# Kernel tuning notes

Hardware: AMD Instinct MI355X
Metric: run time of the kernel (lower is better)

The kernel has to match this reference:

```python
import jax, jax.numpy as jnp
import numpy as np

B, T, D, H, UNITS = 32, 2048, 512, 512, 512

def setup_inputs() -> dict:
    key = jax.random.key(0)
    ks = jax.random.split(key, 5)
    scale = 0.02
    return {
        "features": jax.random.normal(ks[0], (B, T, D), dtype=jnp.float32),
        "hidden": jax.random.normal(ks[1], (B, H), dtype=jnp.float32),
        "Wk": jax.random.normal(ks[2], (D, UNITS), dtype=jnp.float32) * scale,
        "Wb": jnp.zeros((UNITS,), dtype=jnp.float32),
        "Uk": jax.random.normal(ks[3], (H, UNITS), dtype=jnp.float32) * scale,
        "Ub": jnp.zeros((UNITS,), dtype=jnp.float32),
        "Vk": jax.random.normal(ks[4], (UNITS, 1), dtype=jnp.float32) * scale,
        "Vb": jnp.zeros((1,), dtype=jnp.float32),
    }

def reference(features, hidden, Wk, Wb, Uk, Ub, Vk, Vb):
    # features: [B, T, D], hidden: [B, H]
    wf = jnp.einsum('btd,du->btu', features, Wk) + Wb          # [B, T, U]
    uh = (hidden @ Uk + Ub)[:, None, :]                        # [B, 1, U]
    score = jnp.tanh(wf + uh)                                  # [B, T, U]
    logits = jnp.einsum('btu,uo->bto', score, Vk) + Vb         # [B, T, 1]
    attention_weights = jax.nn.softmax(logits, axis=1)         # [B, T, 1]
    context_vector = jnp.sum(attention_weights * features, axis=1)  # [B, D]
    return context_vector, attention_weights
```

## Files before the change

### kernel.cpp

```cpp
#include <hip/hip_runtime.h>
#include <stdint.h>


typedef unsigned short ushort_t;
typedef __attribute__((ext_vector_type(8))) short short8;
typedef __attribute__((ext_vector_type(4))) float f32x4;
typedef __attribute__((ext_vector_type(2))) float float2v;
typedef __attribute__((ext_vector_type(2))) __bf16 bf162v;

#define GLOBAL_AS __attribute__((address_space(1)))
#define LDS_AS    __attribute__((address_space(3)))

__device__ __forceinline__ ushort_t f2bf(float f) {
    uint32_t u = __builtin_bit_cast(uint32_t, f);
    u = (u + 0x7fffu + ((u >> 16) & 1u)) >> 16;
    return (ushort_t)u;
}
__device__ __forceinline__ float bf2f(ushort_t h) {
    uint32_t u = ((uint32_t)h) << 16;
    return __builtin_bit_cast(float, u);
}
__device__ __forceinline__ uint32_t pkbf(float a, float b) {
    bf162v r = __builtin_convertvector((float2v){a, b}, bf162v);
    return __builtin_bit_cast(uint32_t, r);
}

__global__ __launch_bounds__(256) void prep_all(
    const float* __restrict__ feats, ushort_t* __restrict__ fbf,
    const float* __restrict__ hidden, const float* __restrict__ Uk,
    const float* __restrict__ Ub, const float* __restrict__ Wb,
    const float* __restrict__ Wk,
    float* __restrict__ uh, ushort_t* __restrict__ WkT,
    float* __restrict__ ctx_out)
{
    if (blockIdx.x < 16384) {
        const size_t i = ((size_t)blockIdx.x * 256 + threadIdx.x) * 8;
        f32x4 a = *(const f32x4*)(feats + i);
        f32x4 b = *(const f32x4*)(feats + i + 4);
        union { short8 s; uint32_t u[4]; } r;
        r.u[0] = pkbf(a.x, a.y); r.u[1] = pkbf(a.z, a.w);
        r.u[2] = pkbf(b.x, b.y); r.u[3] = pkbf(b.z, b.w);
        *(short8*)(fbf + i) = r.s;
        return;
    }
    const int pb = blockIdx.x - 16384;
    if (pb < 256) {
        const int b  = pb >> 3;
        const int u  = (pb & 7) * 64 + (threadIdx.x & 63);
        const int k0 = (threadIdx.x >> 6) * 128;
        const float* hr = hidden + b * 512;
        float acc = 0.f;
        #pragma unroll 8
        for (int k = k0; k < k0 + 128; ++k)
            acc += hr[k] * Uk[k * 512 + u];
        __shared__ float red[256];
        red[threadIdx.x] = acc;
        __syncthreads();
        if (threadIdx.x < 64) {
            const int ul = threadIdx.x;
            uh[b * 512 + u] = red[ul] + red[ul + 64] + red[ul + 128] + red[ul + 192]
                            + Ub[u] + Wb[u];
        }
    } else if (pb < 512) {
        __shared__ float t[32][33];
        const int blk = pb - 256;
        const int ti = blk >> 4;
        const int tj = blk & 15;
        const int tx = threadIdx.x & 31;
        const int ty = threadIdx.x >> 5;
        #pragma unroll
        for (int q = 0; q < 4; ++q) {
            const int r = ty * 4 + q;
            t[r][tx] = Wk[(ti * 32 + r) * 512 + tj * 32 + tx];
        }
        __syncthreads();
        #pragma unroll
        for (int q = 0; q < 4; ++q) {
            const int r = ty * 4 + q;
            WkT[(tj * 32 + r) * 512 + ti * 32 + tx] = f2bf(t[tx][r]);
        }
    } else {
        ctx_out[(pb - 512) * 256 + threadIdx.x] = 0.f;
    }
}

template<bool CONV>
__global__ __launch_bounds__(512, 4) void attn_gemm(
    const float* __restrict__ afp, const ushort_t* __restrict__ abf,
    const ushort_t* __restrict__ WkT, const float* __restrict__ uh,
    const float* __restrict__ Vk, float* __restrict__ lg4)
{
    __shared__ __align__(16) short As[256 * 32];
    __shared__ __align__(16) short Bs[128 * 32];
    __shared__ float uh_s[128];
    __shared__ float vk_s[128];
    __shared__ float lpart[2][256];

    const int tid  = threadIdx.x;
    const int lane = tid & 63;
    const int quad = lane >> 4;
    const int lc   = lane & 15;
    const int wave = tid >> 6;
    const int wm   = wave >> 1;
    const int wn   = wave & 1;
    const int nc   = (blockIdx.x >> 7) & 3;
    const int mtile= (blockIdx.x & 127) | ((blockIdx.x >> 9) << 7);
    const int m0   = mtile * 256;
    const int bidx = m0 >> 11;

    if (tid < 128) {
        uh_s[tid] = uh[bidx * 512 + nc * 128 + tid];
        vk_s[tid] = Vk[nc * 128 + tid];
    }

    f32x4 acc[4][4];
    #pragma unroll
    for (int tm = 0; tm < 4; ++tm)
        #pragma unroll
        for (int tn = 0; tn < 4; ++tn)
            acc[tm][tn] = (f32x4){0.f, 0.f, 0.f, 0.f};

    for (int ks = 0; ks < 16; ++ks) {
        const int k0 = ks * 32;
        __syncthreads();
        {
            const int row = tid >> 2;
            const int kq  = (tid & 3) * 8;
            const ushort_t* gb = WkT + (size_t)(nc * 128 + row) * 512 + k0 + kq;
            __builtin_amdgcn_global_load_lds(
                (const GLOBAL_AS void*)gb, (LDS_AS void*)(Bs + tid * 8), 16, 0, 0);
        }
        if constexpr (CONV) {
            const int row = tid >> 1;
            const int k16 = (tid & 1) * 16;
            const float* ga = afp + (size_t)(m0 + row) * 512 + k0 + k16;
            f32x4 a0 = *(const f32x4*)(ga);
            f32x4 a1 = *(const f32x4*)(ga + 4);
            f32x4 a2 = *(const f32x4*)(ga + 8);
            f32x4 a3 = *(const f32x4*)(ga + 12);
            union { short8 s; uint32_t u[4]; } r0, r1;
            r0.u[0] = pkbf(a0.x, a0.y); r0.u[1] = pkbf(a0.z, a0.w);
            r0.u[2] = pkbf(a1.x, a1.y); r0.u[3] = pkbf(a1.z, a1.w);
            r1.u[0] = pkbf(a2.x, a2.y); r1.u[1] = pkbf(a2.z, a2.w);
            r1.u[2] = pkbf(a3.x, a3.y); r1.u[3] = pkbf(a3.z, a3.w);
            *(short8*)(As + row * 32 + k16)     = r0.s;
            *(short8*)(As + row * 32 + k16 + 8) = r1.s;
        } else {
            #pragma unroll
            for (int rnd = 0; rnd < 2; ++rnd) {
                const int li  = rnd * 512 + tid;
                const int row = li >> 2;
                const int kq  = (li & 3) * 8;
                const ushort_t* ga = abf + (size_t)(m0 + row) * 512 + k0 + kq;
                __builtin_amdgcn_global_load_lds(
                    (const GLOBAL_AS void*)ga, (LDS_AS void*)(As + li * 8), 16, 0, 0);
            }
        }
        __syncthreads();

        short8 af[4], bfr[4];
        #pragma unroll
        for (int t4 = 0; t4 < 4; ++t4) {
            af[t4]  = *(const short8*)(As + (wm * 64 + t4 * 16 + lc) * 32 + quad * 8);
            bfr[t4] = *(const short8*)(Bs + (wn * 64 + t4 * 16 + lc) * 32 + quad * 8);
        }
        #pragma unroll
        for (int tm = 0; tm < 4; ++tm)
            #pragma unroll
            for (int tn = 0; tn < 4; ++tn)
                acc[tm][tn] = __builtin_amdgcn_mfma_f32_16x16x32_bf16(
                    af[tm], bfr[tn], acc[tm][tn], 0, 0, 0);
    }

    float rp[16];
    #pragma unroll
    for (int i = 0; i < 16; ++i) rp[i] = 0.f;
    #pragma unroll
    for (int tn = 0; tn < 4; ++tn) {
        const int nl  = wn * 64 + tn * 16 + lc;
        const float uhv = uh_s[nl];
        const float vkv = vk_s[nl];
        #pragma unroll
        for (int tm = 0; tm < 4; ++tm)
            #pragma unroll
            for (int i = 0; i < 4; ++i) {
                const float x = acc[tm][tn][i] + uhv;
                const float e = __expf(2.0f * x);
                rp[tm * 4 + i] += (1.0f - 2.0f / (e + 1.0f)) * vkv;
            }
    }
    #pragma unroll
    for (int i = 0; i < 16; ++i) {
        float v = rp[i];
        v += __shfl_xor(v, 1, 64);
        v += __shfl_xor(v, 2, 64);
        v += __shfl_xor(v, 4, 64);
        v += __shfl_xor(v, 8, 64);
        rp[i] = v;
    }
    if (lc == 0) {
        #pragma unroll
        for (int tm = 0; tm < 4; ++tm)
            #pragma unroll
            for (int i = 0; i < 4; ++i)
                lpart[wn][wm * 64 + tm * 16 + quad * 4 + i] = rp[tm * 4 + i];
    }
    __syncthreads();
    if (tid < 256)
        lg4[(size_t)nc * 65536 + m0 + tid] = lpart[0][tid] + lpart[1][tid];
}

__global__ __launch_bounds__(256) void softmax_k(
    const float* __restrict__ lg4, float* __restrict__ aw_out)
{
    const int b = blockIdx.x, tid = threadIdx.x;
    const float* p = lg4 + b * 2048;
    float v[8];
    #pragma unroll
    for (int i = 0; i < 8; ++i) {
        const int idx = tid + i * 256;
        v[i] = p[idx] + p[idx + 65536] + p[idx + 131072] + p[idx + 196608];
    }
    float mx = -1e30f;
    #pragma unroll
    for (int i = 0; i < 8; ++i) mx = fmaxf(mx, v[i]);
    #pragma unroll
    for (int off = 32; off >= 1; off >>= 1) mx = fmaxf(mx, __shfl_xor(mx, off, 64));
    __shared__ float redm[4], reds[4];
    const int wv = tid >> 6, ln = tid & 63;
    if (ln == 0) redm[wv] = mx;
    __syncthreads();
    mx = fmaxf(fmaxf(redm[0], redm[1]), fmaxf(redm[2], redm[3]));
    float s = 0.f;
    #pragma unroll
    for (int i = 0; i < 8; ++i) { v[i] = __expf(v[i] - mx); s += v[i]; }
    #pragma unroll
    for (int off = 32; off >= 1; off >>= 1) s += __shfl_xor(s, off, 64);
    if (ln == 0) reds[wv] = s;
    __syncthreads();
    s = reds[0] + reds[1] + reds[2] + reds[3];
    const float inv = 1.0f / s;
    #pragma unroll
    for (int i = 0; i < 8; ++i)
        aw_out[b * 2048 + tid + i * 256] = v[i] * inv;
}

template<bool BF>
__global__ __launch_bounds__(256) void context_k(
    const ushort_t* __restrict__ fb, const float* __restrict__ ff,
    const float* __restrict__ aw, float* __restrict__ ctx_out)
{
    const int b  = blockIdx.x >> 4;
    const int t0 = (blockIdx.x & 15) * 128 + (threadIdx.x >> 7) * 64;
    const int d4 = (threadIdx.x & 127) * 4;
    const float* wp = aw + b * 2048 + t0;
    f32x4 a = (f32x4){0.f, 0.f, 0.f, 0.f};
    if constexpr (BF) {
        const ushort_t* fp = fb + (size_t)(b * 2048 + t0) * 512 + d4;
        #pragma unroll 4
        for (int tt = 0; tt < 64; ++tt) {
            const float w = wp[tt];
            union { uint2 u2; ushort_t h[4]; } r;
            r.u2 = *(const uint2*)(fp + (size_t)tt * 512);
            a.x += w * bf2f(r.h[0]); a.y += w * bf2f(r.h[1]);
            a.z += w * bf2f(r.h[2]); a.w += w * bf2f(r.h[3]);
        }
    } else {
        const float* fp = ff + (size_t)(b * 2048 + t0) * 512 + d4;
        #pragma unroll 4
        for (int tt = 0; tt < 64; ++tt) {
            const float w = wp[tt];
            const f32x4 f = *(const f32x4*)(fp + (size_t)tt * 512);
            a.x += w * f.x; a.y += w * f.y; a.z += w * f.z; a.w += w * f.w;
        }
    }
    atomicAdd(&ctx_out[b * 512 + d4],     a.x);
    atomicAdd(&ctx_out[b * 512 + d4 + 1], a.y);
    atomicAdd(&ctx_out[b * 512 + d4 + 2], a.z);
    atomicAdd(&ctx_out[b * 512 + d4 + 3], a.w);
}

extern "C" void kernel_launch(void* const* d_in, const int* in_sizes, int n_in,
                              void* d_out, int out_size, void* d_ws, size_t ws_size,
                              hipStream_t stream)
{
    const float* feats  = (const float*)d_in[0];
    const float* hidden = (const float*)d_in[1];
    const float* Wk     = (const float*)d_in[2];
    const float* Wb     = (const float*)d_in[3];
    const float* Uk     = (const float*)d_in[4];
    const float* Ub     = (const float*)d_in[5];
    const float* Vk     = (const float*)d_in[6];

    float* out       = (float*)d_out;
    float* ctx_out_p = out;
    float* aw_out_p  = out + 16384;

    char* ws = (char*)d_ws;
    float*    uh  = (float*)ws;
    ushort_t* WkT = (ushort_t*)(ws + 65536);
    float*    lg4 = (float*)(ws + 589824);
    ushort_t* fbf = (ushort_t*)(ws + (2u << 20));

    const bool bigws = ws_size >= ((2ull << 20) + (64ull << 20));

    if (bigws) {
        prep_all<<<16960, 256, 0, stream>>>(feats, fbf, hidden, Uk, Ub, Wb, Wk,
                                            uh, WkT, ctx_out_p);
        attn_gemm<false><<<1024, 512, 0, stream>>>(feats, fbf, WkT, uh, Vk, lg4);
        softmax_k<<<32,  256, 0, stream>>>(lg4, aw_out_p);
        context_k<true><<<512, 256, 0, stream>>>(fbf, feats, aw_out_p, ctx_out_p);
    } else {
        prep_all<<<16960, 256, 0, stream>>>(feats, (ushort_t*)uh ,
                                            hidden, Uk, Ub, Wb, Wk, uh, WkT,
                                            ctx_out_p);
        attn_gemm<true><<<1024, 512, 0, stream>>>(feats, (const ushort_t*)nullptr,
                                                  WkT, uh, Vk, lg4);
        softmax_k<<<32,  256, 0, stream>>>(lg4, aw_out_p);
        context_k<false><<<512, 256, 0, stream>>>((const ushort_t*)nullptr, feats,
                                                  aw_out_p, ctx_out_p);
    }
}
```

Before: 284.9 us.

## Fuse fp32-to-bf16 conversion into double-buffered full-N GEMM tiles

Drops the separate pass that converted all features to bf16. The GEMM now reads fp32 features and converts them on the fly. Each 1024-thread block covers 128 rows and all 512 units, so features are read once instead of four times and the four-way partial logits reduction goes away. Both A and B tiles are double-buffered so global loads overlap the MFMAs. The costs are higher LDS use per block (about 104 KB, which likely permits only one resident block), a full Wk^T tile reload for every block, and an fp32 feature read in the context kernel.

```diff
diff --git a/kernel.cpp b/kernel.cpp
--- a/kernel.cpp
+++ b/kernel.cpp
@@ -16,34 +16,19 @@
     u = (u + 0x7fffu + ((u >> 16) & 1u)) >> 16;
     return (ushort_t)u;
 }
-__device__ __forceinline__ float bf2f(ushort_t h) {
-    uint32_t u = ((uint32_t)h) << 16;
-    return __builtin_bit_cast(float, u);
-}
 __device__ __forceinline__ uint32_t pkbf(float a, float b) {
     bf162v r = __builtin_convertvector((float2v){a, b}, bf162v);
     return __builtin_bit_cast(uint32_t, r);
 }
 
 __global__ __launch_bounds__(256) void prep_all(
-    const float* __restrict__ feats, ushort_t* __restrict__ fbf,
     const float* __restrict__ hidden, const float* __restrict__ Uk,
     const float* __restrict__ Ub, const float* __restrict__ Wb,
     const float* __restrict__ Wk,
     float* __restrict__ uh, ushort_t* __restrict__ WkT,
     float* __restrict__ ctx_out)
 {
-    if (blockIdx.x < 16384) {
-        const size_t i = ((size_t)blockIdx.x * 256 + threadIdx.x) * 8;
-        f32x4 a = *(const f32x4*)(feats + i);
-        f32x4 b = *(const f32x4*)(feats + i + 4);
-        union { short8 s; uint32_t u[4]; } r;
-        r.u[0] = pkbf(a.x, a.y); r.u[1] = pkbf(a.z, a.w);
-        r.u[2] = pkbf(b.x, b.y); r.u[3] = pkbf(b.z, b.w);
-        *(short8*)(fbf + i) = r.s;
-        return;
-    }
-    const int pb = blockIdx.x - 16384;
+    const int pb = blockIdx.x;
     if (pb < 256) {
         const int b  = pb >> 3;
         const int u  = (pb & 7) * 64 + (threadIdx.x & 63);
@@ -84,34 +69,37 @@
     }
 }
 
-template<bool CONV>
-__global__ __launch_bounds__(512, 4) void attn_gemm(
-    const float* __restrict__ afp, const ushort_t* __restrict__ abf,
-    const ushort_t* __restrict__ WkT, const float* __restrict__ uh,
-    const float* __restrict__ Vk, float* __restrict__ lg4)
-{
-    __shared__ __align__(16) short As[256 * 32];
-    __shared__ __align__(16) short Bs[128 * 32];
-    __shared__ float uh_s[128];
-    __shared__ float vk_s[128];
-    __shared__ float lpart[2][256];
+#define APAD 40
+__global__ __launch_bounds__(1024, 4) void attn_gemm(
+    const float* __restrict__ feats, const ushort_t* __restrict__ WkT,
+    const float* __restrict__ uh, const float* __restrict__ Vk,
+    float* __restrict__ lg)
+{
+    __shared__ __align__(16) short As[2][128 * APAD];
+    __shared__ __align__(16) short Bs[2][512 * 32];
+    __shared__ float uh_s[512];
+    __shared__ float vk_s[512];
+    __shared__ float lpart[8][128];
 
     const int tid  = threadIdx.x;
     const int lane = tid & 63;
     const int quad = lane >> 4;
     const int lc   = lane & 15;
     const int wave = tid >> 6;
-    const int wm   = wave >> 1;
-    const int wn   = wave & 1;
-    const int nc   = (blockIdx.x >> 7) & 3;
-    const int mtile= (blockIdx.x & 127) | ((blockIdx.x >> 9) << 7);
-    const int m0   = mtile * 256;
+    const int wm   = wave >> 3;
+    const int wn   = wave & 7;
+    const int m0   = blockIdx.x * 128;
     const int bidx = m0 >> 11;
 
-    if (tid < 128) {
-        uh_s[tid] = uh[bidx * 512 + nc * 128 + tid];
-        vk_s[tid] = Vk[nc * 128 + tid];
-    }
+    if (tid < 512) {
+        uh_s[tid] = uh[bidx * 512 + tid];
+        vk_s[tid] = Vk[tid];
+    }
+
+    const int rowA = tid >> 3;
+    const int kA   = (tid & 3) * 8;
+    const int kAo  = (tid & 7) * 4;
+    const int rowB = tid >> 2;
 
     f32x4 acc[4][4];
     #pragma unroll
@@ -120,49 +108,49 @@
         for (int tn = 0; tn < 4; ++tn)
             acc[tm][tn] = (f32x4){0.f, 0.f, 0.f, 0.f};
 
+    {
+        #pragma unroll
+        for (int rnd = 0; rnd < 2; ++rnd) {
+            const int li = rnd * 1024 + tid;
+            const int rB = li >> 2;
+            const int kq = (li & 3) * 8;
+            const ushort_t* gb = WkT + (size_t)rB * 512 + kq;
+            __builtin_amdgcn_global_load_lds(
+                (const GLOBAL_AS void*)gb, (LDS_AS void*)(Bs[0] + li * 8), 16, 0, 0);
+        }
+        const f32x4 av = *(const f32x4*)(feats + (size_t)(m0 + rowA) * 512 + kAo);
+        uint2 w;
+        w.x = pkbf(av.x, av.y);
+        w.y = pkbf(av.z, av.w);
+        *(uint2*)(As[0] + rowA * APAD + kAo) = w;
+    }
+
+    int buf = 0;
     for (int ks = 0; ks < 16; ++ks) {
-        const int k0 = ks * 32;
         __syncthreads();
-        {
-            const int row = tid >> 2;
-            const int kq  = (tid & 3) * 8;
-            const ushort_t* gb = WkT + (size_t)(nc * 128 + row) * 512 + k0 + kq;
-            __builtin_amdgcn_global_load_lds(
-                (const GLOBAL_AS void*)gb, (LDS_AS void*)(Bs + tid * 8), 16, 0, 0);
-        }
-        if constexpr (CONV) {
-            const int row = tid >> 1;
-            const int k16 = (tid & 1) * 16;
-            const float* ga = afp + (size_t)(m0 + row) * 512 + k0 + k16;
-            f32x4 a0 = *(const f32x4*)(ga);
-            f32x4 a1 = *(const f32x4*)(ga + 4);
-            f32x4 a2 = *(const f32x4*)(ga + 8);
-            f32x4 a3 = *(const f32x4*)(ga + 12);
-            union { short8 s; uint32_t u[4]; } r0, r1;
-            r0.u[0] = pkbf(a0.x, a0.y); r0.u[1] = pkbf(a0.z, a0.w);
-            r0.u[2] = pkbf(a1.x, a1.y); r0.u[3] = pkbf(a1.z, a1.w);
-            r1.u[0] = pkbf(a2.x, a2.y); r1.u[1] = pkbf(a2.z, a2.w);
-            r1.u[2] = pkbf(a3.x, a3.y); r1.u[3] = pkbf(a3.z, a3.w);
-            *(short8*)(As + row * 32 + k16)     = r0.s;
-            *(short8*)(As + row * 32 + k16 + 8) = r1.s;
-        } else {
+
+        f32x4 a_next;
+        const bool have = (ks + 1) < 16;
+        if (have) {
+            const int k0n = (ks + 1) * 32;
             #pragma unroll
             for (int rnd = 0; rnd < 2; ++rnd) {
-                const int li  = rnd * 512 + tid;
-                const int row = li >> 2;
-                const int kq  = (li & 3) * 8;
-                const ushort_t* ga = abf + (size_t)(m0 + row) * 512 + k0 + kq;
+                const int li = rnd * 1024 + tid;
+                const int rB = li >> 2;
+                const int kq = (li & 3) * 8;
+                const ushort_t* gb = WkT + (size_t)rB * 512 + k0n + kq;
                 __builtin_amdgcn_global_load_lds(
-                    (const GLOBAL_AS void*)ga, (LDS_AS void*)(As + li * 8), 16, 0, 0);
+                    (const GLOBAL_AS void*)gb, (LDS_AS void*)(Bs[buf ^ 1] + li * 8),
+                    16, 0, 0);
             }
-        }
-        __syncthreads();
+            a_next = *(const f32x4*)(feats + (size_t)(m0 + rowA) * 512 + k0n + kAo);
+        }
 
         short8 af[4], bfr[4];
         #pragma unroll
         for (int t4 = 0; t4 < 4; ++t4) {
-            af[t4]  = *(const short8*)(As + (wm * 64 + t4 * 16 + lc) * 32 + quad * 8);
-            bfr[t4] = *(const short8*)(Bs + (wn * 64 + t4 * 16 + lc) * 32 + quad * 8);
+            af[t4]  = *(const short8*)(As[buf] + (wm * 64 + t4 * 16 + lc) * APAD + quad * 8);
+            bfr[t4] = *(const short8*)(Bs[buf] + (wn * 64 + t4 * 16 + lc) * 32 + quad * 8);
         }
         #pragma unroll
         for (int tm = 0; tm < 4; ++tm)
@@ -170,7 +158,16 @@
             for (int tn = 0; tn < 4; ++tn)
                 acc[tm][tn] = __builtin_amdgcn_mfma_f32_16x16x32_bf16(
                     af[tm], bfr[tn], acc[tm][tn], 0, 0, 0);
-    }
+
+        if (have) {
+            uint2 w;
+            w.x = pkbf(a_next.x, a_next.y);
+            w.y = pkbf(a_next.z, a_next.w);
+            *(uint2*)(As[buf ^ 1] + rowA * APAD + kAo) = w;
+        }
+        buf ^= 1;
+    }
+    (void)kA; (void)rowB;
 
     float rp[16];
     #pragma unroll
@@ -206,21 +203,22 @@
                 lpart[wn][wm * 64 + tm * 16 + quad * 4 + i] = rp[tm * 4 + i];
     }
     __syncthreads();
-    if (tid < 256)
-        lg4[(size_t)nc * 65536 + m0 + tid] = lpart[0][tid] + lpart[1][tid];
+    if (tid < 128) {
+        float s = 0.f;
+        #pragma unroll
+        for (int j = 0; j < 8; ++j) s += lpart[j][tid];
+        lg[m0 + tid] = s;
+    }
 }
 
 __global__ __launch_bounds__(256) void softmax_k(
-    const float* __restrict__ lg4, float* __restrict__ aw_out)
+    const float* __restrict__ lg, float* __restrict__ aw_out)
 {
     const int b = blockIdx.x, tid = threadIdx.x;
-    const float* p = lg4 + b * 2048;
+    const float* p = lg + b * 2048;
     float v[8];
     #pragma unroll
-    for (int i = 0; i < 8; ++i) {
-        const int idx = tid + i * 256;
-        v[i] = p[idx] + p[idx + 65536] + p[idx + 131072] + p[idx + 196608];
-    }
+    for (int i = 0; i < 8; ++i) v[i] = p[tid + i * 256];
     float mx = -1e30f;
     #pragma unroll
     for (int i = 0; i < 8; ++i) mx = fmaxf(mx, v[i]);
@@ -245,34 +243,21 @@
         aw_out[b * 2048 + tid + i * 256] = v[i] * inv;
 }
 
-template<bool BF>
 __global__ __launch_bounds__(256) void context_k(
-    const ushort_t* __restrict__ fb, const float* __restrict__ ff,
-    const float* __restrict__ aw, float* __restrict__ ctx_out)
+    const float* __restrict__ feats, const float* __restrict__ aw,
+    float* __restrict__ ctx_out)
 {
     const int b  = blockIdx.x >> 4;
     const int t0 = (blockIdx.x & 15) * 128 + (threadIdx.x >> 7) * 64;
     const int d4 = (threadIdx.x & 127) * 4;
     const float* wp = aw + b * 2048 + t0;
+    const float* fp = feats + (size_t)(b * 2048 + t0) * 512 + d4;
     f32x4 a = (f32x4){0.f, 0.f, 0.f, 0.f};
-    if constexpr (BF) {
-        const ushort_t* fp = fb + (size_t)(b * 2048 + t0) * 512 + d4;
-        #pragma unroll 4
-        for (int tt = 0; tt < 64; ++tt) {
-            const float w = wp[tt];
-            union { uint2 u2; ushort_t h[4]; } r;
-            r.u2 = *(const uint2*)(fp + (size_t)tt * 512);
-            a.x += w * bf2f(r.h[0]); a.y += w * bf2f(r.h[1]);
-            a.z += w * bf2f(r.h[2]); a.w += w * bf2f(r.h[3]);
-        }
-    } else {
-        const float* fp = ff + (size_t)(b * 2048 + t0) * 512 + d4;
-        #pragma unroll 4
-        for (int tt = 0; tt < 64; ++tt) {
-            const float w = wp[tt];
-            const f32x4 f = *(const f32x4*)(fp + (size_t)tt * 512);
-            a.x += w * f.x; a.y += w * f.y; a.z += w * f.z; a.w += w * f.w;
-        }
+    #pragma unroll 4
+    for (int tt = 0; tt < 64; ++tt) {
+        const float w = wp[tt];
+        const f32x4 f = *(const f32x4*)(fp + (size_t)tt * 512);
+        a.x += w * f.x; a.y += w * f.y; a.z += w * f.z; a.w += w * f.w;
     }
     atomicAdd(&ctx_out[b * 512 + d4],     a.x);
     atomicAdd(&ctx_out[b * 512 + d4 + 1], a.y);
@@ -299,25 +284,10 @@
     char* ws = (char*)d_ws;
     float*    uh  = (float*)ws;
     ushort_t* WkT = (ushort_t*)(ws + 65536);
-    float*    lg4 = (float*)(ws + 589824);
-    ushort_t* fbf = (ushort_t*)(ws + (2u << 20));
-
-    const bool bigws = ws_size >= ((2ull << 20) + (64ull << 20));
-
-    if (bigws) {
-        prep_all<<<16960, 256, 0, stream>>>(feats, fbf, hidden, Uk, Ub, Wb, Wk,
-                                            uh, WkT, ctx_out_p);
-        attn_gemm<false><<<1024, 512, 0, stream>>>(feats, fbf, WkT, uh, Vk, lg4);
-        softmax_k<<<32,  256, 0, stream>>>(lg4, aw_out_p);
-        context_k<true><<<512, 256, 0, stream>>>(fbf, feats, aw_out_p, ctx_out_p);
-    } else {
-        prep_all<<<16960, 256, 0, stream>>>(feats, (ushort_t*)uh ,
-                                            hidden, Uk, Ub, Wb, Wk, uh, WkT,
-                                            ctx_out_p);
-        attn_gemm<true><<<1024, 512, 0, stream>>>(feats, (const ushort_t*)nullptr,
-                                                  WkT, uh, Vk, lg4);
-        softmax_k<<<32,  256, 0, stream>>>(lg4, aw_out_p);
-        context_k<false><<<512, 256, 0, stream>>>((const ushort_t*)nullptr, feats,
-                                                  aw_out_p, ctx_out_p);
-    }
-}
+    float*    lg  = (float*)(ws + 589824);
+
+    prep_all <<<576, 256, 0, stream>>>(hidden, Uk, Ub, Wb, Wk, uh, WkT, ctx_out_p);
+    attn_gemm<<<512, 1024, 0, stream>>>(feats, WkT, uh, Vk, lg);
+    softmax_k<<<32,  256, 0, stream>>>(lg, aw_out_p);
+    context_k<<<512, 256, 0, stream>>>(feats, aw_out_p, ctx_out_p);
+}
```

New measurement: 262.3 us. -7.9%, faster.
